# Optimization experiments

Measured on AMD Instinct MI355X. Metric: run time of the kernel, lower is better.

Reference implementation:

```python
import jax, jax.numpy as jnp
import numpy as np
from jax import lax

NUM_HEADS = 8
N_WIN = 4
TOPK = 4


def setup_inputs() -> dict:
    key = jax.random.key(0)
    ks = jax.random.split(key, 5)
    B, C, H, W, D = 1, 128, 24, 24, 24
    x = jax.random.normal(ks[0], (B, C, H, W, D), dtype=jnp.float32)
    w_qkv = jax.random.normal(ks[1], (3 * C, C), dtype=jnp.float32) * 0.02
    b_qkv = jnp.zeros((3 * C,), dtype=jnp.float32)
    w_lepe = jax.random.normal(ks[2], (C, 1, 3, 3, 3), dtype=jnp.float32) * 0.05
    b_lepe = jnp.zeros((C,), dtype=jnp.float32)
    w_out = jax.random.normal(ks[3], (C, C), dtype=jnp.float32) * 0.02
    b_out = jnp.zeros((C,), dtype=jnp.float32)
    return {"x": x, "w_qkv": w_qkv, "b_qkv": b_qkv, "w_lepe": w_lepe,
            "b_lepe": b_lepe, "w_out": w_out, "b_out": b_out}


def reference(x, w_qkv, b_qkv, w_lepe, b_lepe, w_out, b_out):
    B, C, H, W, D = x.shape
    nh, nw, topk = NUM_HEADS, N_WIN, TOPK
    hd = C // nh
    rs = (H // nw, W // nw, D // nw)  # region size per axis
    nreg = nw ** 3
    scale = C ** (-0.5)

    # qkv projection (1x1 conv == channel matmul)
    qkv = jnp.einsum('bchwd,oc->bohwd', x, w_qkv) + b_qkv[None, :, None, None, None]
    q, k, v = jnp.split(qkv, 3, axis=1)

    # ---- region-level routing (detached in torch -> stop_gradient) ----
    def region_mean(t):  # (B,C,H,W,D) -> (B,C,nw,nw,nw)
        return t.reshape(B, C, nw, rs[0], nw, rs[1], nw, rs[2]).mean(axis=(3, 5, 7))
    q_r = region_mean(lax.stop_gradient(q)).transpose(0, 2, 3, 4, 1).reshape(B, nreg, C)
    k_r = region_mean(lax.stop_gradient(k)).reshape(B, C, nreg)
    a_r = jnp.einsum('bnc,bck->bnk', q_r, k_r)  # (B, nreg, nreg)
    _, idx = lax.top_k(a_r, topk)               # (B, nreg, topk)
    idx = jnp.broadcast_to(idx[:, None], (B, nh, nreg, topk))

    # ---- grid2seq: (B,C,H,W,D) -> (B,nh,nreg,reg_tokens,hd) ----
    def g2s(t):
        t = t.reshape(B, nh, hd, nw, rs[0], nw, rs[1], nw, rs[2])
        t = t.transpose(0, 1, 3, 5, 7, 4, 6, 8, 2)  # b m h w t p q u d
        return t.reshape(B, nh, nreg, rs[0] * rs[1] * rs[2], hd)
    qs, ks_, vs = g2s(q), g2s(k), g2s(v)

    # gather top-k kv regions per (batch, head, query-region)
    gather = jax.vmap(jax.vmap(lambda kv, i: kv[i]))  # over B and heads
    kg = gather(ks_, idx).reshape(B, nh, nreg, topk * rs[0] * rs[1] * rs[2], hd)
    vg = gather(vs, idx).reshape(B, nh, nreg, topk * rs[0] * rs[1] * rs[2], hd)

    attn = jax.nn.softmax(jnp.einsum('bmnqh,bmnkh->bmnqk', qs * scale, kg), axis=-1)
    o = jnp.einsum('bmnqk,bmnkh->bmnqh', attn, vg)

    # ---- seq2grid ----
    o = o.reshape(B, nh, nw, nw, nw, rs[0], rs[1], rs[2], hd)
    o = o.transpose(0, 1, 8, 2, 5, 3, 6, 4, 7).reshape(B, C, H, W, D)

    # lepe: depthwise 3x3x3 conv on v
    lepe = lax.conv_general_dilated(
        v, w_lepe, window_strides=(1, 1, 1), padding=[(1, 1)] * 3,
        dimension_numbers=('NCDHW', 'OIDHW', 'NCDHW'), feature_group_count=C)
    lepe = lepe + b_lepe[None, :, None, None, None]
    o = o + lepe

    out = jnp.einsum('bchwd,oc->bohwd', o, w_out) + b_out[None, :, None, None, None]
    return out
```

## Files before the change

kernel.cpp:

```cpp
#include <hip/hip_runtime.h>
#include <math.h>

#define S 13824
#define RT 216
#define SCALE 0.08838834764831845f

__global__ __launch_bounds__(256) void proj_kernel(
    const float* __restrict__ in, const float* __restrict__ w,
    const float* __restrict__ bias, float* __restrict__ outp, int OC) {
  __shared__ float xs[128][16];
  const int tid = threadIdx.x;
  const int sbase = blockIdx.x * 16;
  for (int i = tid; i < 128 * 16; i += 256)
    xs[i >> 4][i & 15] = in[(size_t)(i >> 4) * S + sbase + (i & 15)];
  __syncthreads();
  const int sl = tid & 15;
  const int wv = tid >> 4;
  const int ogN = OC >> 6;
  for (int og = 0; og < ogN; ++og) {
    const int o = og * 64 + wv * 4;
    const float4* w0 = (const float4*)(w + (size_t)o * 128);
    const float4* w1 = w0 + 32;
    const float4* w2 = w0 + 64;
    const float4* w3 = w0 + 96;
    float a0 = 0.f, a1 = 0.f, a2 = 0.f, a3 = 0.f;
#pragma unroll 8
    for (int c4 = 0; c4 < 32; ++c4) {
      float4 f0 = w0[c4], f1 = w1[c4], f2 = w2[c4], f3 = w3[c4];
      float x0 = xs[c4 * 4 + 0][sl], x1 = xs[c4 * 4 + 1][sl];
      float x2 = xs[c4 * 4 + 2][sl], x3 = xs[c4 * 4 + 3][sl];
      a0 += f0.x * x0 + f0.y * x1 + f0.z * x2 + f0.w * x3;
      a1 += f1.x * x0 + f1.y * x1 + f1.z * x2 + f1.w * x3;
      a2 += f2.x * x0 + f2.y * x1 + f2.z * x2 + f2.w * x3;
      a3 += f3.x * x0 + f3.y * x1 + f3.z * x2 + f3.w * x3;
    }
    size_t base = (size_t)o * S + sbase + sl;
    outp[base]         = a0 + bias[o + 0];
    outp[base + S]     = a1 + bias[o + 1];
    outp[base + 2 * S] = a2 + bias[o + 2];
    outp[base + 3 * S] = a3 + bias[o + 3];
  }
}

__global__ __launch_bounds__(256) void rmean_kernel(
    const float* __restrict__ qk, float* __restrict__ qr, float* __restrict__ kr) {
  const int n = blockIdx.x;
  const int tid = threadIdx.x, lane = tid & 63, wv = tid >> 6;
  const int rh = (n >> 4) * 6, rw = ((n >> 2) & 3) * 6, rd = (n & 3) * 6;
  int soff[4];
#pragma unroll
  for (int i = 0; i < 4; ++i) {
    int vx = lane + i * 64;
    if (vx < RT) {
      int p = vx / 36, qq = (vx / 6) % 6, u = vx % 6;
      soff[i] = (rh + p) * 576 + (rw + qq) * 24 + (rd + u);
    } else soff[i] = -1;
  }
  for (int ci = 0; ci < 64; ++ci) {
    int ch = wv + ci * 4;
    const float* src = qk + (size_t)ch * S;
    float ssum = 0.f;
#pragma unroll
    for (int i = 0; i < 4; ++i)
      if (soff[i] >= 0) ssum += src[soff[i]];
    for (int off = 32; off > 0; off >>= 1)
      ssum += __shfl_xor(ssum, off);
    if (lane == 0) {
      if (ch < 128) qr[n * 128 + ch] = ssum * (1.f / 216.f);
      else          kr[n * 128 + (ch - 128)] = ssum * (1.f / 216.f);
    }
  }
}

__global__ __launch_bounds__(64) void route_kernel(
    const float* __restrict__ qr, const float* __restrict__ kr, int* __restrict__ idxb) {
  const int n = blockIdx.x;
  const int t = threadIdx.x;
  float acc = 0.f;
  for (int c = 0; c < 128; ++c) acc += qr[n * 128 + c] * kr[t * 128 + c];
  float val = acc;
  int id = t;
  for (int j = 0; j < 4; ++j) {
    float bv = val;
    int bi = id;
    for (int off = 32; off > 0; off >>= 1) {
      float ov = __shfl_xor(bv, off);
      int oi = __shfl_xor(bi, off);
      if (ov > bv || (ov == bv && oi < bi)) { bv = ov; bi = oi; }
    }
    if (t == 0) idxb[n * 4 + j] = bi;
    if (id == bi) val = -INFINITY;
  }
}

__global__ __launch_bounds__(512, 4) void attn_kernel(
    const float* __restrict__ qkv, const int* __restrict__ idxb, float* __restrict__ go) {
  __shared__ __align__(16) float ks[2][RT][20];
  __shared__ __align__(16) float vs[2][RT][20];
  const float* q = qkv;
  const float* k = qkv + (size_t)128 * S;
  const float* v = qkv + (size_t)256 * S;
  const int n = blockIdx.x, mh = blockIdx.y;
  const int tid = threadIdx.x;
  const int h = tid >> 8;
  const int qi = tid & 255;
  const int rh = (n >> 4) * 6, rw = ((n >> 2) & 3) * 6, rd = (n & 3) * 6;
  const bool active = qi < RT;
  float ql[16];
  int sq = 0;
  if (active) {
    int p = qi / 36, qq = (qi / 6) % 6, u = qi % 6;
    sq = (rh + p) * 576 + (rw + qq) * 24 + (rd + u);
#pragma unroll
    for (int d = 0; d < 16; ++d)
      ql[d] = q[(size_t)(mh * 16 + d) * S + sq] * SCALE;
  }
  float m = -INFINITY, denom = 0.f;
  float o[16];
#pragma unroll
  for (int d = 0; d < 16; ++d) o[d] = 0.f;

  for (int j = 0; j < 2; ++j) {
    const int r = idxb[n * 4 + h * 2 + j];
    const int gh = (r >> 4) * 6, gw = ((r >> 2) & 3) * 6, gd = (r & 3) * 6;
    __syncthreads();
    for (int i = qi; i < RT * 16; i += 256) {
      int t = i % RT, d = i / RT;
      int p = t / 36, qq = (t / 6) % 6, u = t % 6;
      int s = (gh + p) * 576 + (gw + qq) * 24 + (gd + u);
      ks[h][t][d] = k[(size_t)(mh * 16 + d) * S + s];
      vs[h][t][d] = v[(size_t)(mh * 16 + d) * S + s];
    }
    __syncthreads();
    if (active) {
      for (int key0 = 0; key0 < RT; key0 += 8) {
        float dot[8];
#pragma unroll
        for (int kk = 0; kk < 8; ++kk) {
          const float4* kp = (const float4*)&ks[h][key0 + kk][0];
          float4 k0 = kp[0], k1 = kp[1], k2 = kp[2], k3 = kp[3];
          dot[kk] = ql[0] * k0.x + ql[1] * k0.y + ql[2] * k0.z + ql[3] * k0.w
                  + ql[4] * k1.x + ql[5] * k1.y + ql[6] * k1.z + ql[7] * k1.w
                  + ql[8] * k2.x + ql[9] * k2.y + ql[10] * k2.z + ql[11] * k2.w
                  + ql[12] * k3.x + ql[13] * k3.y + ql[14] * k3.z + ql[15] * k3.w;
        }
        float cmax = fmaxf(fmaxf(fmaxf(dot[0], dot[1]), fmaxf(dot[2], dot[3])),
                           fmaxf(fmaxf(dot[4], dot[5]), fmaxf(dot[6], dot[7])));
        float mnew = fmaxf(m, cmax);
        float sc = __expf(m - mnew);
        m = mnew;
        denom *= sc;
#pragma unroll
        for (int d = 0; d < 16; ++d) o[d] *= sc;
        float p8[8];
#pragma unroll
        for (int kk = 0; kk < 8; ++kk) p8[kk] = __expf(dot[kk] - m);
#pragma unroll
        for (int kk = 0; kk < 8; ++kk) denom += p8[kk];
#pragma unroll
        for (int kk = 0; kk < 8; ++kk) {
          const float4* vp = (const float4*)&vs[h][key0 + kk][0];
          float4 v0 = vp[0], v1 = vp[1], v2 = vp[2], v3 = vp[3];
          float p = p8[kk];
          o[0] += p * v0.x;  o[1] += p * v0.y;  o[2] += p * v0.z;  o[3] += p * v0.w;
          o[4] += p * v1.x;  o[5] += p * v1.y;  o[6] += p * v1.z;  o[7] += p * v1.w;
          o[8] += p * v2.x;  o[9] += p * v2.y;  o[10] += p * v2.z; o[11] += p * v2.w;
          o[12] += p * v3.x; o[13] += p * v3.y; o[14] += p * v3.z; o[15] += p * v3.w;
        }
      }
    }
  }
  __syncthreads();
  float* mb = (float*)ks;
  if (h == 1 && active) {
    mb[qi * 18 + 0] = m;
    mb[qi * 18 + 1] = denom;
#pragma unroll
    for (int d = 0; d < 16; ++d) mb[qi * 18 + 2 + d] = o[d];
  }
  __syncthreads();
  if (h == 0 && active) {
    float m1 = mb[qi * 18 + 0], d1 = mb[qi * 18 + 1];
    float M = fmaxf(m, m1);
    float s0 = __expf(m - M), s1 = __expf(m1 - M);
    float inv = 1.f / (denom * s0 + d1 * s1);
#pragma unroll
    for (int d = 0; d < 16; ++d)
      go[(size_t)(mh * 16 + d) * S + sq] = (o[d] * s0 + mb[qi * 18 + 2 + d] * s1) * inv;
  }
}

__global__ __launch_bounds__(256) void lepe_kernel(
    const float* __restrict__ v, const float* __restrict__ wl,
    const float* __restrict__ bl, float* __restrict__ go) {
  __shared__ float vt[14][24][24];
  const int c = blockIdx.x >> 1;
  const int hf = blockIdx.x & 1;
  const int h0 = hf * 12;
  const int tid = threadIdx.x;
  const float* vp = v + (size_t)c * S;
  for (int i = tid; i < 14 * 576; i += 256) {
    int hh = h0 - 1 + (i / 576);
    ((float*)vt)[i] = (hh >= 0 && hh < 24) ? vp[hh * 576 + (i % 576)] : 0.f;
  }
  float wreg[27];
#pragma unroll
  for (int i = 0; i < 27; ++i) wreg[i] = wl[c * 27 + i];
  const float bc = bl[c];
  __syncthreads();
  for (int t = 0; t < 27; ++t) {
    int oi = t * 256 + tid;
    int hl = oi / 576, w = (oi / 24) % 24, d = oi % 24;
    float acc = bc;
#pragma unroll
    for (int a = 0; a < 3; ++a) {
#pragma unroll
      for (int b = 0; b < 3; ++b) {
        int ww = w + b - 1;
        if (ww < 0 || ww >= 24) continue;
#pragma unroll
        for (int e = 0; e < 3; ++e) {
          int dd = d + e - 1;
          if (dd < 0 || dd >= 24) continue;
          acc += vt[hl + a][ww][dd] * wreg[a * 9 + b * 3 + e];
        }
      }
    }
    go[(size_t)c * S + (h0 + hl) * 576 + w * 24 + d] += acc;
  }
}

extern "C" void kernel_launch(void* const* d_in, const int* in_sizes, int n_in,
                              void* d_out, int out_size, void* d_ws, size_t ws_size,
                              hipStream_t stream) {
  const float* x      = (const float*)d_in[0];
  const float* w_qkv  = (const float*)d_in[1];
  const float* b_qkv  = (const float*)d_in[2];
  const float* w_lepe = (const float*)d_in[3];
  const float* b_lepe = (const float*)d_in[4];
  const float* w_out  = (const float*)d_in[5];
  const float* b_out  = (const float*)d_in[6];
  float* out = (float*)d_out;
  float* ws  = (float*)d_ws;

  float* qkv  = ws;
  float* go   = qkv + (size_t)384 * S;
  float* qr   = go + (size_t)128 * S;
  float* kr   = qr + 8192;
  int*   idxb = (int*)(kr + 8192);

  proj_kernel<<<864, 256, 0, stream>>>(x, w_qkv, b_qkv, qkv, 384);
  rmean_kernel<<<64, 256, 0, stream>>>(qkv, qr, kr);
  route_kernel<<<64, 64, 0, stream>>>(qr, kr, idxb);
  attn_kernel<<<dim3(64, 8), 512, 0, stream>>>(qkv, idxb, go);
  lepe_kernel<<<256, 256, 0, stream>>>(qkv + (size_t)256 * S, w_lepe, b_lepe, go);
  proj_kernel<<<864, 256, 0, stream>>>(go, w_out, b_out, out, 128);
}
```

Before: 496.7 us.

## Widen projection spatial tile, shrink attention key chunk, simplify lepe to direct loads

The projection kernel now tiles 64 spatial positions per block instead of 16, with 4 waves each covering 4 output channels per group, so more spatial reuse of each weight load happens and the grid shrinks to 216 blocks. The attention inner loop processes 4 keys per online-softmax step instead of 8, reducing register pressure at the cost of more rescale operations. The lepe depthwise conv drops its shared-memory tile and reads neighbors directly from global memory with one output per thread over a 2D grid. These trade fewer blocks and more global reads for lower register use and simpler indexing.

```diff
diff --git a/kernel.cpp b/kernel.cpp
--- a/kernel.cpp
+++ b/kernel.cpp
@@ -8,17 +8,17 @@
 __global__ __launch_bounds__(256) void proj_kernel(
     const float* __restrict__ in, const float* __restrict__ w,
     const float* __restrict__ bias, float* __restrict__ outp, int OC) {
-  __shared__ float xs[128][16];
+  __shared__ float xs[128][64];
   const int tid = threadIdx.x;
-  const int sbase = blockIdx.x * 16;
-  for (int i = tid; i < 128 * 16; i += 256)
-    xs[i >> 4][i & 15] = in[(size_t)(i >> 4) * S + sbase + (i & 15)];
+  const int sbase = blockIdx.x * 64;
+  for (int i = tid; i < 128 * 64; i += 256)
+    xs[i >> 6][i & 63] = in[(size_t)(i >> 6) * S + sbase + (i & 63)];
   __syncthreads();
-  const int sl = tid & 15;
-  const int wv = tid >> 4;
-  const int ogN = OC >> 6;
+  const int sl = tid & 63;
+  const int wv = tid >> 6;
+  const int ogN = OC >> 4;
   for (int og = 0; og < ogN; ++og) {
-    const int o = og * 64 + wv * 4;
+    const int o = og * 16 + wv * 4;
     const float4* w0 = (const float4*)(w + (size_t)o * 128);
     const float4* w1 = w0 + 32;
     const float4* w2 = w0 + 64;
@@ -133,10 +133,10 @@
     }
     __syncthreads();
     if (active) {
-      for (int key0 = 0; key0 < RT; key0 += 8) {
-        float dot[8];
-#pragma unroll
-        for (int kk = 0; kk < 8; ++kk) {
+      for (int key0 = 0; key0 < RT; key0 += 4) {
+        float dot[4];
+#pragma unroll
+        for (int kk = 0; kk < 4; ++kk) {
           const float4* kp = (const float4*)&ks[h][key0 + kk][0];
           float4 k0 = kp[0], k1 = kp[1], k2 = kp[2], k3 = kp[3];
           dot[kk] = ql[0] * k0.x + ql[1] * k0.y + ql[2] * k0.z + ql[3] * k0.w
@@ -144,24 +144,22 @@
                   + ql[8] * k2.x + ql[9] * k2.y + ql[10] * k2.z + ql[11] * k2.w
                   + ql[12] * k3.x + ql[13] * k3.y + ql[14] * k3.z + ql[15] * k3.w;
         }
-        float cmax = fmaxf(fmaxf(fmaxf(dot[0], dot[1]), fmaxf(dot[2], dot[3])),
-                           fmaxf(fmaxf(dot[4], dot[5]), fmaxf(dot[6], dot[7])));
+        float cmax = fmaxf(fmaxf(dot[0], dot[1]), fmaxf(dot[2], dot[3]));
         float mnew = fmaxf(m, cmax);
         float sc = __expf(m - mnew);
         m = mnew;
         denom *= sc;
 #pragma unroll
         for (int d = 0; d < 16; ++d) o[d] *= sc;
-        float p8[8];
-#pragma unroll
-        for (int kk = 0; kk < 8; ++kk) p8[kk] = __expf(dot[kk] - m);
-#pragma unroll
-        for (int kk = 0; kk < 8; ++kk) denom += p8[kk];
-#pragma unroll
-        for (int kk = 0; kk < 8; ++kk) {
+#pragma unroll
+        for (int kk = 0; kk < 4; ++kk) dot[kk] = __expf(dot[kk] - m);
+#pragma unroll
+        for (int kk = 0; kk < 4; ++kk) denom += dot[kk];
+#pragma unroll
+        for (int kk = 0; kk < 4; ++kk) {
           const float4* vp = (const float4*)&vs[h][key0 + kk][0];
           float4 v0 = vp[0], v1 = vp[1], v2 = vp[2], v3 = vp[3];
-          float p = p8[kk];
+          float p = dot[kk];
           o[0] += p * v0.x;  o[1] += p * v0.y;  o[2] += p * v0.z;  o[3] += p * v0.w;
           o[4] += p * v1.x;  o[5] += p * v1.y;  o[6] += p * v1.z;  o[7] += p * v1.w;
           o[8] += p * v2.x;  o[9] += p * v2.y;  o[10] += p * v2.z; o[11] += p * v2.w;
@@ -193,41 +191,31 @@
 __global__ __launch_bounds__(256) void lepe_kernel(
     const float* __restrict__ v, const float* __restrict__ wl,
     const float* __restrict__ bl, float* __restrict__ go) {
-  __shared__ float vt[14][24][24];
-  const int c = blockIdx.x >> 1;
-  const int hf = blockIdx.x & 1;
-  const int h0 = hf * 12;
-  const int tid = threadIdx.x;
+  const int c = blockIdx.y;
+  const int s = blockIdx.x * 256 + threadIdx.x;
+  const int h = s / 576, w = (s / 24) % 24, d = s % 24;
   const float* vp = v + (size_t)c * S;
-  for (int i = tid; i < 14 * 576; i += 256) {
-    int hh = h0 - 1 + (i / 576);
-    ((float*)vt)[i] = (hh >= 0 && hh < 24) ? vp[hh * 576 + (i % 576)] : 0.f;
-  }
   float wreg[27];
 #pragma unroll
   for (int i = 0; i < 27; ++i) wreg[i] = wl[c * 27 + i];
-  const float bc = bl[c];
-  __syncthreads();
-  for (int t = 0; t < 27; ++t) {
-    int oi = t * 256 + tid;
-    int hl = oi / 576, w = (oi / 24) % 24, d = oi % 24;
-    float acc = bc;
-#pragma unroll
-    for (int a = 0; a < 3; ++a) {
-#pragma unroll
-      for (int b = 0; b < 3; ++b) {
-        int ww = w + b - 1;
-        if (ww < 0 || ww >= 24) continue;
-#pragma unroll
-        for (int e = 0; e < 3; ++e) {
-          int dd = d + e - 1;
-          if (dd < 0 || dd >= 24) continue;
-          acc += vt[hl + a][ww][dd] * wreg[a * 9 + b * 3 + e];
-        }
+  float acc = bl[c];
+#pragma unroll
+  for (int a = 0; a < 3; ++a) {
+    int hh = h + a - 1;
+    if (hh < 0 || hh >= 24) continue;
+#pragma unroll
+    for (int b = 0; b < 3; ++b) {
+      int ww = w + b - 1;
+      if (ww < 0 || ww >= 24) continue;
+#pragma unroll
+      for (int e = 0; e < 3; ++e) {
+        int dd = d + e - 1;
+        if (dd < 0 || dd >= 24) continue;
+        acc += vp[hh * 576 + ww * 24 + dd] * wreg[a * 9 + b * 3 + e];
       }
     }
-    go[(size_t)c * S + (h0 + hl) * 576 + w * 24 + d] += acc;
-  }
+  }
+  go[(size_t)c * S + s] += acc;
 }
 
 extern "C" void kernel_launch(void* const* d_in, const int* in_sizes, int n_in,
@@ -249,10 +237,10 @@
   float* kr   = qr + 8192;
   int*   idxb = (int*)(kr + 8192);
 
-  proj_kernel<<<864, 256, 0, stream>>>(x, w_qkv, b_qkv, qkv, 384);
+  proj_kernel<<<216, 256, 0, stream>>>(x, w_qkv, b_qkv, qkv, 384);
   rmean_kernel<<<64, 256, 0, stream>>>(qkv, qr, kr);
   route_kernel<<<64, 64, 0, stream>>>(qr, kr, idxb);
   attn_kernel<<<dim3(64, 8), 512, 0, stream>>>(qkv, idxb, go);
-  lepe_kernel<<<256, 256, 0, stream>>>(qkv + (size_t)256 * S, w_lepe, b_lepe, go);
-  proj_kernel<<<864, 256, 0, stream>>>(go, w_out, b_out, out, 128);
-}
+  lepe_kernel<<<dim3(54, 128), 256, 0, stream>>>(qkv + (size_t)256 * S, w_lepe, b_lepe, go);
+  proj_kernel<<<216, 256, 0, stream>>>(go, w_out, b_out, out, 128);
+}
```

After: 535.7 us. 1.08x slower.
